# Optimization experiments

Hardware: AMD Instinct MI355X
Metric: run time of the kernel (lower is better)

The kernel has to match this reference:

```python
import jax, jax.numpy as jnp
import numpy as np

N_NODES = 100000
N_EDGES = 625000
NODE_DIM = 128
N_REL = 16
SLOPE = 0.2


def setup_inputs() -> dict:
    key = jax.random.key(0)
    k1, k2, k3, k4 = jax.random.split(key, 4)
    x_base = jax.random.normal(k1, (N_NODES, NODE_DIM), dtype=jnp.float32)
    # xavier-uniform-like init for a_r_params [n_rel, 2*node_dim]
    limit = float(np.sqrt(6.0 / (N_REL + 2 * NODE_DIM)))
    a_r_params = jax.random.uniform(k2, (N_REL, 2 * NODE_DIM), dtype=jnp.float32,
                                    minval=-limit, maxval=limit)
    rel_edge_index = jax.random.randint(k3, (2, N_EDGES), 0, N_NODES, dtype=jnp.int64 if jax.config.jax_enable_x64 else jnp.int32).astype(jnp.int32)
    rel_edge_type = jax.random.randint(k4, (N_EDGES,), 0, N_REL).astype(jnp.int32)
    return {"x_base": x_base, "a_r_params": a_r_params,
            "rel_edge_index": rel_edge_index, "rel_edge_type": rel_edge_type}


def reference(x_base, a_r_params, rel_edge_index, rel_edge_type):
    n_nodes, d = x_base.shape
    src = rel_edge_index[0]
    dst = rel_edge_index[1]
    # gather per-edge node features and per-edge relation params
    x_u = x_base[src]                       # [E, d]
    x_v = x_base[dst]                       # [E, d]
    a_r = a_r_params[rel_edge_type]         # [E, 2d]
    # sum(a_r * cat([x_u, x_v])) without materializing the concat
    e = jnp.sum(a_r[:, :d] * x_u, axis=-1) + jnp.sum(a_r[:, d:] * x_v, axis=-1)  # [E]
    e_act = jnp.where(e >= 0, e, SLOPE * e)  # leaky relu
    # scatter softmax over src groups (stable: subtract per-segment max)
    seg_max = jax.ops.segment_max(e_act, src, num_segments=n_nodes)  # [N]
    ex = jnp.exp(e_act - seg_max[src])
    seg_sum = jax.ops.segment_sum(ex, src, num_segments=n_nodes)     # [N]
    alpha = ex / seg_sum[src]
    return alpha
```

## Files before the change

kernel.cpp:

```cpp
#include <hip/hip_runtime.h>
#include <hip/hip_fp16.h>

#define NN 100000
#define NE 625000
#define ND 128
#define NR 16
#define SLOPE 0.2f
#define PAD 132
#define NB 782
#define CAP 1280
#define MAXE 5
#define PRE_BLOCKS 1563
#define SC_EPB 8192
#define SC_BLOCKS 77

__global__ void zero_cursor(unsigned* __restrict__ c) {
    int i = blockIdx.x * 256 + threadIdx.x;
    if (i < NB) c[i] = 0u;
}

__global__ __launch_bounds__(256) void pre_scatter(
        const float* __restrict__ x, const float* __restrict__ a,
        const int* __restrict__ srcs, const int* __restrict__ dsts,
        const int* __restrict__ etype,
        __half* __restrict__ table, int2* __restrict__ bedge,
        unsigned* __restrict__ cursor) {
    __shared__ float xs[64 * PAD];
    int tid = threadIdx.x;
    int b = blockIdx.x;

    if (b >= SC_BLOCKS) {
        int blockBase = (b - SC_BLOCKS) * 64;
#pragma unroll
        for (int i = 0; i < 8; ++i) {
            int f = tid + i * 256;
            int row = f >> 5;
            int col = (f & 31) << 2;
            size_t g = (size_t)blockBase * ND + (size_t)f * 4;
            float4 v = (g < (size_t)NN * ND) ? *(const float4*)&x[g]
                                             : make_float4(0.f, 0.f, 0.f, 0.f);
            *(float4*)&xs[row * PAD + col] = v;
        }
        __syncthreads();

        int q  = __builtin_amdgcn_readfirstlane(tid >> 6);
        int nl = tid & 63;
        int n  = blockBase + nl;
        if (n >= NN) return;

        const float* arow = a + (size_t)((q & 1) * 8) * 256 + (q >> 1) * 128;
        float acc[8];
#pragma unroll
        for (int j = 0; j < 8; ++j) acc[j] = 0.0f;

        const float* xr = &xs[nl * PAD];
        for (int k = 0; k < ND; k += 4) {
            float4 xv = *(const float4*)&xr[k];
#pragma unroll
            for (int j = 0; j < 8; ++j) {
                float4 av = *(const float4*)&arow[(size_t)j * 256 + k];
                acc[j] += av.x * xv.x + av.y * xv.y + av.z * xv.z + av.w * xv.w;
            }
        }
        __half2 hv[4];
#pragma unroll
        for (int p = 0; p < 4; ++p)
            hv[p] = __floats2half2_rn(acc[p * 2], acc[p * 2 + 1]);
        *(uint4*)(table + (size_t)n * 32 + q * 8) = *(uint4*)hv;
    } else {
        unsigned* hist = (unsigned*)xs;
        for (int j = tid; j < NB; j += 256) hist[j] = 0u;
        __syncthreads();

        int base = b * SC_EPB;
#pragma unroll
        for (int i = 0; i < 8; ++i) {
            int e = base + (i * 256 + tid) * 4;
            if (e < NE) {
                int4 s4 = *(const int4*)&srcs[e];
                atomicAdd(&hist[s4.x >> 7], 1u);
                atomicAdd(&hist[s4.y >> 7], 1u);
                atomicAdd(&hist[s4.z >> 7], 1u);
                atomicAdd(&hist[s4.w >> 7], 1u);
            }
        }
        __syncthreads();
        for (int j = tid; j < NB; j += 256) {
            unsigned c = hist[j];
            hist[j] = c ? atomicAdd(&cursor[j], c) : 0u;
        }
        __syncthreads();
#pragma unroll
        for (int i = 0; i < 8; ++i) {
            int e = base + (i * 256 + tid) * 4;
            if (e < NE) {
                int4 s4 = *(const int4*)&srcs[e];
                int4 d4 = *(const int4*)&dsts[e];
                int4 r4 = *(const int4*)&etype[e];
                int ss[4] = {s4.x, s4.y, s4.z, s4.w};
                int dd[4] = {d4.x, d4.y, d4.z, d4.w};
                int rr[4] = {r4.x, r4.y, r4.z, r4.w};
#pragma unroll
                for (int j = 0; j < 4; ++j) {
                    int bk = ss[j] >> 7;
                    unsigned slot = atomicAdd(&hist[bk], 1u);
                    if (slot < CAP) {
                        int w0 = (ss[j] & 127) | (rr[j] << 7) | (dd[j] << 11);
                        bedge[(size_t)bk * CAP + slot] = make_int2(w0, e + j);
                    }
                }
            }
        }
    }
}

__global__ __launch_bounds__(256) void fused_abc(
        const unsigned* __restrict__ cursor, const int2* __restrict__ bedge,
        const __half* __restrict__ table, float* __restrict__ out) {
    __shared__ float lsum[128];
    int b = blockIdx.x;
    int tid = threadIdx.x;
    if (tid < 128) lsum[tid] = 0.f;
    __syncthreads();

    unsigned count = cursor[b];
    if (count > CAP) count = CAP;
    const int2* bin = bedge + (size_t)b * CAP;

    int2 ed[MAXE];
    float u[MAXE], v[MAXE], ex[MAXE];

#pragma unroll
    for (int k = 0; k < MAXE; ++k) {
        unsigned i = tid + 256u * k;
        if (i < count) ed[k] = bin[i];
    }
#pragma unroll
    for (int k = 0; k < MAXE; ++k) {
        unsigned i = tid + 256u * k;
        if (i < count) {
            int w = ed[k].x;
            int sl = w & 127;
            int r  = (w >> 7) & 15;
            int d  = w >> 11;
            u[k] = __half2float(table[(size_t)((b << 7) + sl) * 32 + r]);
            v[k] = __half2float(table[(size_t)d * 32 + 16 + r]);
        }
    }
#pragma unroll
    for (int k = 0; k < MAXE; ++k) {
        unsigned i = tid + 256u * k;
        if (i < count) {
            float av = u[k] + v[k];
            av = (av >= 0.f) ? av : SLOPE * av;
            ex[k] = __expf(av);
            atomicAdd(&lsum[ed[k].x & 127], ex[k]);
        }
    }
    __syncthreads();
#pragma unroll
    for (int k = 0; k < MAXE; ++k) {
        unsigned i = tid + 256u * k;
        if (i < count)
            out[ed[k].y] = __fdividef(ex[k], lsum[ed[k].x & 127]);
    }
}

extern "C" void kernel_launch(void* const* d_in, const int* in_sizes, int n_in,
                              void* d_out, int out_size, void* d_ws, size_t ws_size,
                              hipStream_t stream) {
    const float* x     = (const float*)d_in[0];
    const float* a     = (const float*)d_in[1];
    const int*   eidx  = (const int*)d_in[2];
    const int*   etype = (const int*)d_in[3];
    const int*   srcs  = eidx;
    const int*   dsts  = eidx + NE;
    float*       out   = (float*)d_out;

    char* ws = (char*)d_ws;
    __half*   table  = (__half*)(ws);
    int2*     bedge  = (int2*)(ws + 6400000);
    unsigned* cursor = (unsigned*)(ws + 14407680);

    dim3 blk(256);
    zero_cursor<<<dim3(4), blk, 0, stream>>>(cursor);
    pre_scatter<<<dim3(PRE_BLOCKS + SC_BLOCKS), blk, 0, stream>>>(
        x, a, srcs, dsts, etype, table, bedge, cursor);
    fused_abc<<<dim3(NB), blk, 0, stream>>>(cursor, bedge, table, out);
}
```

Baseline: 53.55 us.

## Compute node-relation projection table with split-bf16 MFMA and halve scatter block size

```diff
diff --git a/kernel.cpp b/kernel.cpp
--- a/kernel.cpp
+++ b/kernel.cpp
@@ -6,17 +6,27 @@
 #define ND 128
 #define NR 16
 #define SLOPE 0.2f
-#define PAD 132
 #define NB 782
 #define CAP 1280
 #define MAXE 5
 #define PRE_BLOCKS 1563
-#define SC_EPB 8192
-#define SC_BLOCKS 77
+#define SC_EPB 4096
+#define SC_BLOCKS 153
+#define LSTR 136
+
+using s16x8 = __attribute__((ext_vector_type(8))) short;
+using f32x4 = __attribute__((ext_vector_type(4))) float;
 
 __global__ void zero_cursor(unsigned* __restrict__ c) {
     int i = blockIdx.x * 256 + threadIdx.x;
     if (i < NB) c[i] = 0u;
+}
+
+__device__ __forceinline__ void bf_split(float x, unsigned short& h, unsigned short& l) {
+    unsigned u = __float_as_uint(x);
+    h = (unsigned short)(u >> 16);
+    float hf = __uint_as_float(u & 0xFFFF0000u);
+    l = (unsigned short)(__float_as_uint(x - hf) >> 16);
 }
 
 __global__ __launch_bounds__(256) void pre_scatter(
@@ -25,56 +35,100 @@
         const int* __restrict__ etype,
         __half* __restrict__ table, int2* __restrict__ bedge,
         unsigned* __restrict__ cursor) {
-    __shared__ float xs[64 * PAD];
+    __shared__ __align__(16) unsigned short smem[4 * 16 + 64 * LSTR * 2 + 32 * LSTR * 2];
     int tid = threadIdx.x;
     int b = blockIdx.x;
 
     if (b >= SC_BLOCKS) {
-        int blockBase = (b - SC_BLOCKS) * 64;
+        unsigned short* Xh = smem;
+        unsigned short* Xl = Xh + 64 * LSTR;
+        unsigned short* Wh = Xl + 64 * LSTR;
+        unsigned short* Wl = Wh + 32 * LSTR;
+        int nb = (b - SC_BLOCKS) * 64;
+
 #pragma unroll
         for (int i = 0; i < 8; ++i) {
             int f = tid + i * 256;
             int row = f >> 5;
-            int col = (f & 31) << 2;
-            size_t g = (size_t)blockBase * ND + (size_t)f * 4;
+            int c4 = (f & 31) << 2;
+            size_t g = (size_t)nb * ND + (size_t)f * 4;
             float4 v = (g < (size_t)NN * ND) ? *(const float4*)&x[g]
                                              : make_float4(0.f, 0.f, 0.f, 0.f);
-            *(float4*)&xs[row * PAD + col] = v;
-        }
-        __syncthreads();
-
-        int q  = __builtin_amdgcn_readfirstlane(tid >> 6);
-        int nl = tid & 63;
-        int n  = blockBase + nl;
-        if (n >= NN) return;
-
-        const float* arow = a + (size_t)((q & 1) * 8) * 256 + (q >> 1) * 128;
-        float acc[8];
-#pragma unroll
-        for (int j = 0; j < 8; ++j) acc[j] = 0.0f;
-
-        const float* xr = &xs[nl * PAD];
-        for (int k = 0; k < ND; k += 4) {
-            float4 xv = *(const float4*)&xr[k];
-#pragma unroll
-            for (int j = 0; j < 8; ++j) {
-                float4 av = *(const float4*)&arow[(size_t)j * 256 + k];
-                acc[j] += av.x * xv.x + av.y * xv.y + av.z * xv.z + av.w * xv.w;
+            unsigned short h0, l0, h1, l1, h2, l2, h3, l3;
+            bf_split(v.x, h0, l0); bf_split(v.y, h1, l1);
+            bf_split(v.z, h2, l2); bf_split(v.w, h3, l3);
+            *(uint2*)&Xh[row * LSTR + c4] =
+                make_uint2((unsigned)h0 | ((unsigned)h1 << 16),
+                           (unsigned)h2 | ((unsigned)h3 << 16));
+            *(uint2*)&Xl[row * LSTR + c4] =
+                make_uint2((unsigned)l0 | ((unsigned)l1 << 16),
+                           (unsigned)l2 | ((unsigned)l3 << 16));
+        }
+#pragma unroll
+        for (int i = 0; i < 4; ++i) {
+            int f = tid + i * 256;
+            int row = f >> 6;
+            int c4 = f & 63;
+            int o = row + ((c4 >> 5) << 4);
+            int k = (c4 & 31) << 2;
+            float4 v = *(const float4*)&a[(size_t)row * 256 + (size_t)c4 * 4];
+            unsigned short h0, l0, h1, l1, h2, l2, h3, l3;
+            bf_split(v.x, h0, l0); bf_split(v.y, h1, l1);
+            bf_split(v.z, h2, l2); bf_split(v.w, h3, l3);
+            *(uint2*)&Wh[o * LSTR + k] =
+                make_uint2((unsigned)h0 | ((unsigned)h1 << 16),
+                           (unsigned)h2 | ((unsigned)h3 << 16));
+            *(uint2*)&Wl[o * LSTR + k] =
+                make_uint2((unsigned)l0 | ((unsigned)l1 << 16),
+                           (unsigned)l2 | ((unsigned)l3 << 16));
+        }
+        __syncthreads();
+
+        int w = tid >> 6;
+        int lane = tid & 63;
+        int r16 = lane & 15;
+        int q = lane >> 4;
+
+        f32x4 acc0 = {0.f, 0.f, 0.f, 0.f};
+        f32x4 acc1 = {0.f, 0.f, 0.f, 0.f};
+        const unsigned short* xh = &Xh[(w * 16 + r16) * LSTR + q * 8];
+        const unsigned short* xl = &Xl[(w * 16 + r16) * LSTR + q * 8];
+        const unsigned short* w0h = &Wh[r16 * LSTR + q * 8];
+        const unsigned short* w0l = &Wl[r16 * LSTR + q * 8];
+        const unsigned short* w1h = &Wh[(16 + r16) * LSTR + q * 8];
+        const unsigned short* w1l = &Wl[(16 + r16) * LSTR + q * 8];
+#pragma unroll
+        for (int ks = 0; ks < 4; ++ks) {
+            s16x8 ah = *(const s16x8*)&xh[ks * 32];
+            s16x8 al = *(const s16x8*)&xl[ks * 32];
+            s16x8 bh0 = *(const s16x8*)&w0h[ks * 32];
+            s16x8 bl0 = *(const s16x8*)&w0l[ks * 32];
+            s16x8 bh1 = *(const s16x8*)&w1h[ks * 32];
+            s16x8 bl1 = *(const s16x8*)&w1l[ks * 32];
+            acc0 = __builtin_amdgcn_mfma_f32_16x16x32_bf16(ah, bh0, acc0, 0, 0, 0);
+            acc0 = __builtin_amdgcn_mfma_f32_16x16x32_bf16(al, bh0, acc0, 0, 0, 0);
+            acc0 = __builtin_amdgcn_mfma_f32_16x16x32_bf16(ah, bl0, acc0, 0, 0, 0);
+            acc1 = __builtin_amdgcn_mfma_f32_16x16x32_bf16(ah, bh1, acc1, 0, 0, 0);
+            acc1 = __builtin_amdgcn_mfma_f32_16x16x32_bf16(al, bh1, acc1, 0, 0, 0);
+            acc1 = __builtin_amdgcn_mfma_f32_16x16x32_bf16(ah, bl1, acc1, 0, 0, 0);
+        }
+        int nrow = nb + w * 16 + q * 4;
+#pragma unroll
+        for (int r = 0; r < 4; ++r) {
+            int n = nrow + r;
+            if (n < NN) {
+                table[(size_t)n * 32 + r16]      = __float2half_rn(acc0[r]);
+                table[(size_t)n * 32 + 16 + r16] = __float2half_rn(acc1[r]);
             }
         }
-        __half2 hv[4];
-#pragma unroll
-        for (int p = 0; p < 4; ++p)
-            hv[p] = __floats2half2_rn(acc[p * 2], acc[p * 2 + 1]);
-        *(uint4*)(table + (size_t)n * 32 + q * 8) = *(uint4*)hv;
     } else {
-        unsigned* hist = (unsigned*)xs;
+        unsigned* hist = (unsigned*)smem;
         for (int j = tid; j < NB; j += 256) hist[j] = 0u;
         __syncthreads();
 
         int base = b * SC_EPB;
 #pragma unroll
-        for (int i = 0; i < 8; ++i) {
+        for (int i = 0; i < 4; ++i) {
             int e = base + (i * 256 + tid) * 4;
             if (e < NE) {
                 int4 s4 = *(const int4*)&srcs[e];
@@ -91,7 +145,7 @@
         }
         __syncthreads();
 #pragma unroll
-        for (int i = 0; i < 8; ++i) {
+        for (int i = 0; i < 4; ++i) {
             int e = base + (i * 256 + tid) * 4;
             if (e < NE) {
                 int4 s4 = *(const int4*)&srcs[e];
```

Result: faster. 45.87 us (-14.3%).
